# Performance work log

Hardware: AMD Instinct MI355X
Metric: run time of the kernel (lower is better)

The kernel has to match this reference:

```python
import jax, jax.numpy as jnp
import numpy as np

B, T, C, H = 4, 2048, 1024, 16
D = C // H  # head dim = 64

def setup_inputs() -> dict:
    key = jax.random.key(0)
    ks = jax.random.split(key, 5)
    s = 0.02
    return {
        "x": jax.random.normal(ks[0], (B, T, C), dtype=jnp.float32),
        # torch Linear convention: weight shape (out, in), y = x @ W.T + b
        "Wqkv": jax.random.normal(ks[1], (3 * C, C), dtype=jnp.float32) * s,
        "bqkv": jax.random.normal(ks[2], (3 * C,), dtype=jnp.float32) * s,
        "Wproj": jax.random.normal(ks[3], (C, C), dtype=jnp.float32) * s,
        "bproj": jax.random.normal(ks[4], (C,), dtype=jnp.float32) * s,
    }

def reference(x, Wqkv, bqkv, Wproj, bproj):
    b, t, c = x.shape
    qkv = x @ Wqkv.T + bqkv                      # [B,T,3C]
    q, k, v = jnp.split(qkv, 3, axis=-1)
    # [B,T,C] -> [B,H,T,D]
    q = q.reshape(b, t, H, D).transpose(0, 2, 1, 3)
    k = k.reshape(b, t, H, D).transpose(0, 2, 1, 3)
    v = v.reshape(b, t, H, D).transpose(0, 2, 1, 3)
    scale = 1.0 / jnp.sqrt(jnp.float32(D))
    att = jnp.einsum('bhqd,bhkd->bhqk', q, k) * scale   # [B,H,T,T]
    # additive causal mask: -inf strictly above diagonal
    mask = jnp.triu(jnp.full((t, t), -jnp.inf, dtype=att.dtype), k=1)
    att = att + mask
    att = jax.nn.softmax(att, axis=-1)
    # dropout p=0.0 -> identity
    y = jnp.einsum('bhqk,bhkd->bhqd', att, v)            # [B,H,T,D]
    y = y.transpose(0, 2, 1, 3).reshape(b, t, c)         # [B,T,C]
    y = y @ Wproj.T + bproj
    return y
```

## Files before the change

kernel.cpp:

```cpp
#include <hip/hip_runtime.h>
#include <hip/hip_bf16.h>
#include <stdint.h>

constexpr int BB = 4, TT = 2048, CC = 1024, HH = 16, DD = 64;

typedef __bf16 bf16_t;
typedef bf16_t bf16x8 __attribute__((ext_vector_type(8)));
typedef float f32x4 __attribute__((ext_vector_type(4)));

__device__ __forceinline__ unsigned short f2bf(float f) {
    union { __bf16 h; unsigned short u; } v;
    v.h = (__bf16)f;
    return v.u;
}

__device__ __forceinline__ f32x4 mfma16(bf16x8 a, bf16x8 b, f32x4 c) {
    return __builtin_amdgcn_mfma_f32_16x16x32_bf16(a, b, c, 0, 0, 0);
}

#define LOAD_LDS16(g, l)                                                      \
    __builtin_amdgcn_global_load_lds(                                         \
        (const __attribute__((address_space(1))) void*)(g),                   \
        (__attribute__((address_space(3))) void*)(l), 16, 0, 0)

__global__ __launch_bounds__(256) void cvt_bf16(const float* __restrict__ in,
                                                unsigned short* __restrict__ out,
                                                long n) {
    long i = ((long)blockIdx.x * blockDim.x + threadIdx.x) * 4;
    long stride = (long)gridDim.x * blockDim.x * 4;
    for (; i < n; i += stride) {
        float4 v = *(const float4*)(in + i);
        ushort4 o;
        o.x = f2bf(v.x); o.y = f2bf(v.y); o.z = f2bf(v.z); o.w = f2bf(v.w);
        *(ushort4*)(out + i) = o;
    }
}

template <int MODE>
__global__ __launch_bounds__(256, 2) void gemm_bt(
    const unsigned short* __restrict__ A,
    const unsigned short* __restrict__ Bw,
    const float* __restrict__ bias,
    unsigned short* __restrict__ qb, unsigned short* __restrict__ kb,
    unsigned short* __restrict__ vtb, float* __restrict__ outf,
    int M, int N, int K) {
    __shared__ unsigned short As[2][128 * 32];
    __shared__ unsigned short Bs[2][128 * 32];
    const int tid = threadIdx.x;
    const int w = tid >> 6, lane = tid & 63;
    const int g = lane >> 4, q16 = lane & 15;
    const int wr = w >> 1, wc = w & 1;
    const int mbase = blockIdx.x * 128;
    const int nbase = blockIdx.y * 128;
    const int srow = lane >> 2;
    const int scol = (lane & 3) * 8;

    f32x4 acc[4][4];
#pragma unroll
    for (int i = 0; i < 4; ++i)
#pragma unroll
        for (int j = 0; j < 4; ++j) acc[i][j] = (f32x4){0.f, 0.f, 0.f, 0.f};

    const int nk = K >> 5;

    auto stage = [&](int buf, int t) {
        const int k0 = t << 5;
#pragma unroll
        for (int ii = 0; ii < 2; ++ii) {
            const int i = w + ii * 4;
            const unsigned short* ga =
                A + (long)(mbase + i * 16 + srow) * K + k0 + scol;
            LOAD_LDS16(ga, &As[buf][i * 512]);
            const unsigned short* gb =
                Bw + (long)(nbase + i * 16 + srow) * K + k0 + scol;
            LOAD_LDS16(gb, &Bs[buf][i * 512]);
        }
    };

    stage(0, 0);
    __syncthreads();
    int cur = 0;
    for (int t = 0; t < nk; ++t) {
        if (t + 1 < nk) stage(cur ^ 1, t + 1);
        bf16x8 af[4], bfr[4];
#pragma unroll
        for (int mi = 0; mi < 4; ++mi)
            af[mi] = *(const bf16x8*)&As[cur][(wr * 64 + mi * 16 + q16) * 32 + 8 * g];
#pragma unroll
        for (int ni = 0; ni < 4; ++ni)
            bfr[ni] = *(const bf16x8*)&Bs[cur][(wc * 64 + ni * 16 + q16) * 32 + 8 * g];
#pragma unroll
        for (int mi = 0; mi < 4; ++mi)
#pragma unroll
            for (int ni = 0; ni < 4; ++ni)
                acc[mi][ni] = mfma16(af[mi], bfr[ni], acc[mi][ni]);
        __syncthreads();
        cur ^= 1;
    }

#pragma unroll
    for (int mi = 0; mi < 4; ++mi) {
#pragma unroll
        for (int ni = 0; ni < 4; ++ni) {
            const int n = nbase + wc * 64 + ni * 16 + q16;
            const float bv = bias[n];
#pragma unroll
            for (int r = 0; r < 4; ++r) {
                const int m = mbase + wr * 64 + mi * 16 + 4 * g + r;
                const float val = acc[mi][ni][r] + bv;
                if (MODE == 0) {
                    const int which = n >> 10, rem = n & 1023;
                    const int h = rem >> 6, d = rem & 63;
                    const int b = m >> 11, t = m & 2047;
                    const long bh = (long)(b * HH + h);
                    if (which == 0)
                        qb[(bh * TT + t) * DD + d] = f2bf(val * 0.125f);
                    else if (which == 1)
                        kb[(bh * TT + t) * DD + d] = f2bf(val);
                    else
                        vtb[(bh * DD + d) * TT + t] = f2bf(val);
                } else {
                    outf[(long)m * N + n] = val;
                }
            }
        }
    }
}

__global__ __launch_bounds__(256, 4) void attn_fwd(
    const unsigned short* __restrict__ qb, const unsigned short* __restrict__ kb,
    const unsigned short* __restrict__ vtb, unsigned short* __restrict__ attb) {
    __shared__ __align__(16) unsigned short Ks[2][64 * 64];
    __shared__ __align__(16) unsigned short Vs[2][64 * 64];
    __shared__ __align__(16) unsigned short plds[4][16 * 64];
    const int tid = threadIdx.x;
    const int w = tid >> 6, lane = tid & 63;
    const int g = lane >> 4, q16 = lane & 15;
    const int bid = blockIdx.x;
    const int swz = (bid & 7) * 256 + (bid >> 3);
    const int bx = swz & 31, bh = swz >> 5;
    const int b = bh >> 4, h = bh & 15;
    const int qbase = bx * 64 + w * 16;

    const unsigned short* Q = qb + (long)bh * TT * DD;
    const unsigned short* Kp = kb + (long)bh * TT * DD;
    const unsigned short* Vt = vtb + (long)bh * DD * TT;

    const int srow = tid >> 3;
    const int ssl = ((tid & 7) ^ (srow & 7)) * 8;
    unsigned short* kdst0 = &Ks[0][0] + w * 512;
    unsigned short* vdst0 = &Vs[0][0] + w * 512;

    auto stageKV = [&](int buf, int kt) {
        const long kb0 = (long)kt * 64;
        const unsigned short* gk = Kp + (kb0 + srow) * DD + ssl;
        const unsigned short* gv = Vt + (long)srow * TT + kb0 + ssl;
        unsigned short* kd = kdst0 + buf * 4096;
        unsigned short* vd = vdst0 + buf * 4096;
        LOAD_LDS16(gk, kd);
        LOAD_LDS16(gk + 32l * DD, kd + 2048);
        LOAD_LDS16(gv, vd);
        LOAD_LDS16(gv + 32l * TT, vd + 2048);
    };

    bf16x8 aq0 = *(const bf16x8*)&Q[(qbase + q16) * DD + 8 * g];
    bf16x8 aq1 = *(const bf16x8*)&Q[(qbase + q16) * DD + 32 + 8 * g];

    f32x4 acc[4];
#pragma unroll
    for (int i = 0; i < 4; ++i) acc[i] = (f32x4){0.f, 0.f, 0.f, 0.f};
    float mrow = -1e30f, lrow = 0.f;

    const int slot0 = (g ^ (q16 & 7)) << 3;
    const int nkt = bx + 1;
    stageKV(0, 0);
    __syncthreads();
    int cur = 0;
    for (int kt = 0; kt < nkt; ++kt) {
        if (kt + 1 < nkt) stageKV(cur ^ 1, kt + 1);
        const int kbase = kt * 64;
        f32x4 p[4];
#pragma unroll
        for (int s = 0; s < 4; ++s) p[s] = (f32x4){0.f, 0.f, 0.f, 0.f};
#pragma unroll
        for (int s = 0; s < 4; ++s) {
            const int kr = (16 * s + q16) * 64;
            bf16x8 bk0 = *(const bf16x8*)&Ks[cur][kr + slot0];
            bf16x8 bk1 = *(const bf16x8*)&Ks[cur][kr + (slot0 ^ 32)];
            p[s] = mfma16(bk0, aq0, p[s]);
            p[s] = mfma16(bk1, aq1, p[s]);
        }
        const int q = qbase + q16;
        if (kt == nkt - 1) {
#pragma unroll
            for (int s = 0; s < 4; ++s)
#pragma unroll
                for (int r = 0; r < 4; ++r)
                    if (kbase + 16 * s + 4 * g + r > q) p[s][r] = -1e30f;
        }
        float t = fmaxf(fmaxf(p[0][0], p[0][1]), fmaxf(p[0][2], p[0][3]));
#pragma unroll
        for (int s = 1; s < 4; ++s)
            t = fmaxf(t, fmaxf(fmaxf(p[s][0], p[s][1]), fmaxf(p[s][2], p[s][3])));
        t = fmaxf(t, __shfl_xor(t, 16));
        t = fmaxf(t, __shfl_xor(t, 32));
        if (__all(t - mrow <= 8.0f)) {
            float ssum = 0.f;
#pragma unroll
            for (int s = 0; s < 4; ++s)
#pragma unroll
                for (int r = 0; r < 4; ++r) {
                    p[s][r] = __expf(p[s][r] - mrow);
                    ssum += p[s][r];
                }
            ssum += __shfl_xor(ssum, 16);
            ssum += __shfl_xor(ssum, 32);
            lrow += ssum;
        } else {
            const float nm = fmaxf(mrow, t);
            const float fs = __expf(mrow - nm);
            mrow = nm;
            float ssum = 0.f;
#pragma unroll
            for (int s = 0; s < 4; ++s)
#pragma unroll
                for (int r = 0; r < 4; ++r) {
                    p[s][r] = __expf(p[s][r] - nm);
                    ssum += p[s][r];
                }
            ssum += __shfl_xor(ssum, 16);
            ssum += __shfl_xor(ssum, 32);
            lrow = lrow * fs + ssum;
            float fr[4];
#pragma unroll
            for (int r = 0; r < 4; ++r) fr[r] = __shfl(fs, 4 * g + r);
#pragma unroll
            for (int ni = 0; ni < 4; ++ni)
#pragma unroll
                for (int r = 0; r < 4; ++r) acc[ni][r] *= fr[r];
        }
#pragma unroll
        for (int s = 0; s < 4; ++s) {
            ushort4 pk;
            pk.x = f2bf(p[s][0]); pk.y = f2bf(p[s][1]);
            pk.z = f2bf(p[s][2]); pk.w = f2bf(p[s][3]);
            const int Gp = ((2 * s + (g >> 1)) ^ (q16 & 7)) * 8 + (g & 1) * 4;
            *(ushort4*)&plds[w][q16 * 64 + Gp] = pk;
        }
        bf16x8 pa0 = *(const bf16x8*)&plds[w][q16 * 64 + slot0];
        bf16x8 pa1 = *(const bf16x8*)&plds[w][q16 * 64 + (slot0 ^ 32)];
#pragma unroll
        for (int ni = 0; ni < 4; ++ni) {
            const int vr = (ni * 16 + q16) * 64;
            bf16x8 bv0 = *(const bf16x8*)&Vs[cur][vr + slot0];
            bf16x8 bv1 = *(const bf16x8*)&Vs[cur][vr + (slot0 ^ 32)];
            acc[ni] = mfma16(pa0, bv0, acc[ni]);
            acc[ni] = mfma16(pa1, bv1, acc[ni]);
        }
        __syncthreads();
        cur ^= 1;
    }
    float inv[4];
#pragma unroll
    for (int r = 0; r < 4; ++r) inv[r] = 1.0f / __shfl(lrow, 4 * g + r);
#pragma unroll
    for (int ni = 0; ni < 4; ++ni)
#pragma unroll
        for (int r = 0; r < 4; ++r) {
            const int q = qbase + 4 * g + r;
            const int d = ni * 16 + q16;
            attb[(((long)b * TT + q) * HH + h) * DD + d] =
                f2bf(acc[ni][r] * inv[r]);
        }
}

extern "C" void kernel_launch(void* const* d_in, const int* in_sizes, int n_in,
                              void* d_out, int out_size, void* d_ws, size_t ws_size,
                              hipStream_t stream) {
    const float* x = (const float*)d_in[0];
    const float* Wqkv = (const float*)d_in[1];
    const float* bqkv = (const float*)d_in[2];
    const float* Wproj = (const float*)d_in[3];
    const float* bproj = (const float*)d_in[4];
    float* out = (float*)d_out;

    char* ws = (char*)d_ws;
    unsigned short* xb = (unsigned short*)(ws);
    unsigned short* wqkvb = (unsigned short*)(ws + (16l << 20));
    unsigned short* wprojb = (unsigned short*)(ws + (22l << 20));
    unsigned short* qb = (unsigned short*)(ws + (24l << 20));
    unsigned short* kb = (unsigned short*)(ws + (40l << 20));
    unsigned short* vtb = (unsigned short*)(ws + (56l << 20));
    unsigned short* attb = xb;

    cvt_bf16<<<2048, 256, 0, stream>>>(x, xb, (long)BB * TT * CC);
    cvt_bf16<<<2048, 256, 0, stream>>>(Wqkv, wqkvb, (long)3 * CC * CC);
    cvt_bf16<<<1024, 256, 0, stream>>>(Wproj, wprojb, (long)CC * CC);

    gemm_bt<0><<<dim3(64, 24), 256, 0, stream>>>(xb, wqkvb, bqkv, qb, kb, vtb,
                                                 nullptr, BB * TT, 3 * CC, CC);
    attn_fwd<<<2048, 256, 0, stream>>>(qb, kb, vtb, attb);
    gemm_bt<1><<<dim3(64, 8), 256, 0, stream>>>(attb, wprojb, bproj, nullptr,
                                                nullptr, nullptr, out, BB * TT,
                                                CC, CC);
}
```

Measured before the change: 218.9 us.

## Double attention query tile per block, merge conversion kernels, add MFMA priority hints

Each attention block now handles 128 query rows, with each wave owning two 16-row sub-tiles. Every staged K/V tile is therefore reused by twice as many queries, and the grid is halved. The causal mask is now applied per sub-tile whenever the key block crosses the diagonal. The three fp32-to-bf16 conversion launches are merged into one kernel that dispatches by index range, and s_setprio is raised around the MFMA sections. The larger tile costs more registers and gives coarser causal load balance, since the longest blocks now do twice the work.

```diff
diff --git a/kernel.cpp b/kernel.cpp
--- a/kernel.cpp
+++ b/kernel.cpp
@@ -23,16 +23,26 @@
         (const __attribute__((address_space(1))) void*)(g),                   \
         (__attribute__((address_space(3))) void*)(l), 16, 0, 0)
 
-__global__ __launch_bounds__(256) void cvt_bf16(const float* __restrict__ in,
-                                                unsigned short* __restrict__ out,
-                                                long n) {
-    long i = ((long)blockIdx.x * blockDim.x + threadIdx.x) * 4;
-    long stride = (long)gridDim.x * blockDim.x * 4;
-    for (; i < n; i += stride) {
-        float4 v = *(const float4*)(in + i);
+__global__ __launch_bounds__(256) void cvt_all(
+    const float* __restrict__ a, long na,
+    const float* __restrict__ b, long nb,
+    const float* __restrict__ c, long nc,
+    unsigned short* __restrict__ oa, unsigned short* __restrict__ ob,
+    unsigned short* __restrict__ oc) {
+    const long ntot = na + nb + nc;
+    long i = (long)blockIdx.x * blockDim.x + threadIdx.x;
+    const long stride = (long)gridDim.x * blockDim.x;
+    for (; i < ntot; i += stride) {
+        const float* src;
+        unsigned short* dst;
+        long q = i;
+        if (q < na) { src = a; dst = oa; }
+        else if (q < na + nb) { q -= na; src = b; dst = ob; }
+        else { q -= na + nb; src = c; dst = oc; }
+        float4 v = *(const float4*)(src + q * 4);
         ushort4 o;
         o.x = f2bf(v.x); o.y = f2bf(v.y); o.z = f2bf(v.z); o.w = f2bf(v.w);
-        *(ushort4*)(out + i) = o;
+        *(ushort4*)(dst + q * 4) = o;
     }
 }
 
@@ -137,10 +147,10 @@
     const int w = tid >> 6, lane = tid & 63;
     const int g = lane >> 4, q16 = lane & 15;
     const int bid = blockIdx.x;
-    const int swz = (bid & 7) * 256 + (bid >> 3);
-    const int bx = swz & 31, bh = swz >> 5;
+    const int swz = (bid & 7) * 128 + (bid >> 3);
+    const int bx = swz & 15, bh = swz >> 4;
     const int b = bh >> 4, h = bh & 15;
-    const int qbase = bx * 64 + w * 16;
+    const int qbase = bx * 128 + w * 32;
 
     const unsigned short* Q = qb + (long)bh * TT * DD;
     const unsigned short* Kp = kb + (long)bh * TT * DD;
@@ -163,115 +173,132 @@
         LOAD_LDS16(gv + 32l * TT, vd + 2048);
     };
 
-    bf16x8 aq0 = *(const bf16x8*)&Q[(qbase + q16) * DD + 8 * g];
-    bf16x8 aq1 = *(const bf16x8*)&Q[(qbase + q16) * DD + 32 + 8 * g];
-
-    f32x4 acc[4];
-#pragma unroll
-    for (int i = 0; i < 4; ++i) acc[i] = (f32x4){0.f, 0.f, 0.f, 0.f};
-    float mrow = -1e30f, lrow = 0.f;
+    bf16x8 aq[2][2];
+#pragma unroll
+    for (int js = 0; js < 2; ++js) {
+        aq[js][0] = *(const bf16x8*)&Q[(qbase + js * 16 + q16) * DD + 8 * g];
+        aq[js][1] = *(const bf16x8*)&Q[(qbase + js * 16 + q16) * DD + 32 + 8 * g];
+    }
+
+    f32x4 acc[2][4];
+#pragma unroll
+    for (int js = 0; js < 2; ++js)
+#pragma unroll
+        for (int i = 0; i < 4; ++i) acc[js][i] = (f32x4){0.f, 0.f, 0.f, 0.f};
+    float mrow[2] = {-1e30f, -1e30f}, lrow[2] = {0.f, 0.f};
 
     const int slot0 = (g ^ (q16 & 7)) << 3;
-    const int nkt = bx + 1;
+    const int nkt = 2 * bx + 2;
     stageKV(0, 0);
     __syncthreads();
     int cur = 0;
     for (int kt = 0; kt < nkt; ++kt) {
         if (kt + 1 < nkt) stageKV(cur ^ 1, kt + 1);
         const int kbase = kt * 64;
-        f32x4 p[4];
-#pragma unroll
-        for (int s = 0; s < 4; ++s) p[s] = (f32x4){0.f, 0.f, 0.f, 0.f};
-#pragma unroll
-        for (int s = 0; s < 4; ++s) {
-            const int kr = (16 * s + q16) * 64;
-            bf16x8 bk0 = *(const bf16x8*)&Ks[cur][kr + slot0];
-            bf16x8 bk1 = *(const bf16x8*)&Ks[cur][kr + (slot0 ^ 32)];
-            p[s] = mfma16(bk0, aq0, p[s]);
-            p[s] = mfma16(bk1, aq1, p[s]);
-        }
-        const int q = qbase + q16;
-        if (kt == nkt - 1) {
-#pragma unroll
-            for (int s = 0; s < 4; ++s)
-#pragma unroll
-                for (int r = 0; r < 4; ++r)
-                    if (kbase + 16 * s + 4 * g + r > q) p[s][r] = -1e30f;
-        }
-        float t = fmaxf(fmaxf(p[0][0], p[0][1]), fmaxf(p[0][2], p[0][3]));
-#pragma unroll
-        for (int s = 1; s < 4; ++s)
-            t = fmaxf(t, fmaxf(fmaxf(p[s][0], p[s][1]), fmaxf(p[s][2], p[s][3])));
-        t = fmaxf(t, __shfl_xor(t, 16));
-        t = fmaxf(t, __shfl_xor(t, 32));
-        if (__all(t - mrow <= 8.0f)) {
-            float ssum = 0.f;
-#pragma unroll
-            for (int s = 0; s < 4; ++s)
-#pragma unroll
-                for (int r = 0; r < 4; ++r) {
-                    p[s][r] = __expf(p[s][r] - mrow);
-                    ssum += p[s][r];
-                }
-            ssum += __shfl_xor(ssum, 16);
-            ssum += __shfl_xor(ssum, 32);
-            lrow += ssum;
-        } else {
-            const float nm = fmaxf(mrow, t);
-            const float fs = __expf(mrow - nm);
-            mrow = nm;
-            float ssum = 0.f;
-#pragma unroll
-            for (int s = 0; s < 4; ++s)
-#pragma unroll
-                for (int r = 0; r < 4; ++r) {
-                    p[s][r] = __expf(p[s][r] - nm);
-                    ssum += p[s][r];
-                }
-            ssum += __shfl_xor(ssum, 16);
-            ssum += __shfl_xor(ssum, 32);
-            lrow = lrow * fs + ssum;
-            float fr[4];
-#pragma unroll
-            for (int r = 0; r < 4; ++r) fr[r] = __shfl(fs, 4 * g + r);
-#pragma unroll
-            for (int ni = 0; ni < 4; ++ni)
-#pragma unroll
-                for (int r = 0; r < 4; ++r) acc[ni][r] *= fr[r];
-        }
-#pragma unroll
-        for (int s = 0; s < 4; ++s) {
-            ushort4 pk;
-            pk.x = f2bf(p[s][0]); pk.y = f2bf(p[s][1]);
-            pk.z = f2bf(p[s][2]); pk.w = f2bf(p[s][3]);
-            const int Gp = ((2 * s + (g >> 1)) ^ (q16 & 7)) * 8 + (g & 1) * 4;
-            *(ushort4*)&plds[w][q16 * 64 + Gp] = pk;
-        }
-        bf16x8 pa0 = *(const bf16x8*)&plds[w][q16 * 64 + slot0];
-        bf16x8 pa1 = *(const bf16x8*)&plds[w][q16 * 64 + (slot0 ^ 32)];
-#pragma unroll
-        for (int ni = 0; ni < 4; ++ni) {
-            const int vr = (ni * 16 + q16) * 64;
-            bf16x8 bv0 = *(const bf16x8*)&Vs[cur][vr + slot0];
-            bf16x8 bv1 = *(const bf16x8*)&Vs[cur][vr + (slot0 ^ 32)];
-            acc[ni] = mfma16(pa0, bv0, acc[ni]);
-            acc[ni] = mfma16(pa1, bv1, acc[ni]);
+#pragma unroll
+        for (int js = 0; js < 2; ++js) {
+            f32x4 p[4];
+#pragma unroll
+            for (int s = 0; s < 4; ++s) p[s] = (f32x4){0.f, 0.f, 0.f, 0.f};
+            __builtin_amdgcn_s_setprio(1);
+#pragma unroll
+            for (int s = 0; s < 4; ++s) {
+                const int kr = (16 * s + q16) * 64;
+                bf16x8 bk0 = *(const bf16x8*)&Ks[cur][kr + slot0];
+                bf16x8 bk1 = *(const bf16x8*)&Ks[cur][kr + (slot0 ^ 32)];
+                p[s] = mfma16(bk0, aq[js][0], p[s]);
+                p[s] = mfma16(bk1, aq[js][1], p[s]);
+            }
+            __builtin_amdgcn_s_setprio(0);
+            const int qset = qbase + js * 16;
+            if (kbase + 63 > qset) {
+                const int q = qset + q16;
+#pragma unroll
+                for (int s = 0; s < 4; ++s)
+#pragma unroll
+                    for (int r = 0; r < 4; ++r)
+                        if (kbase + 16 * s + 4 * g + r > q) p[s][r] = -1e30f;
+            }
+            float t = fmaxf(fmaxf(p[0][0], p[0][1]), fmaxf(p[0][2], p[0][3]));
+#pragma unroll
+            for (int s = 1; s < 4; ++s)
+                t = fmaxf(t, fmaxf(fmaxf(p[s][0], p[s][1]), fmaxf(p[s][2], p[s][3])));
+            t = fmaxf(t, __shfl_xor(t, 16));
+            t = fmaxf(t, __shfl_xor(t, 32));
+            if (__all(t - mrow[js] <= 8.0f)) {
+                float ssum = 0.f;
+#pragma unroll
+                for (int s = 0; s < 4; ++s)
+#pragma unroll
+                    for (int r = 0; r < 4; ++r) {
+                        p[s][r] = __expf(p[s][r] - mrow[js]);
+                        ssum += p[s][r];
+                    }
+                ssum += __shfl_xor(ssum, 16);
+                ssum += __shfl_xor(ssum, 32);
+                lrow[js] += ssum;
+            } else {
+                const float nm = fmaxf(mrow[js], t);
+                const float fs = __expf(mrow[js] - nm);
+                mrow[js] = nm;
+                float ssum = 0.f;
+#pragma unroll
+                for (int s = 0; s < 4; ++s)
+#pragma unroll
+                    for (int r = 0; r < 4; ++r) {
+                        p[s][r] = __expf(p[s][r] - nm);
+                        ssum += p[s][r];
+                    }
+                ssum += __shfl_xor(ssum, 16);
+                ssum += __shfl_xor(ssum, 32);
+                lrow[js] = lrow[js] * fs + ssum;
+                float fr[4];
+#pragma unroll
+                for (int r = 0; r < 4; ++r) fr[r] = __shfl(fs, 4 * g + r);
+#pragma unroll
+                for (int ni = 0; ni < 4; ++ni)
+#pragma unroll
+                    for (int r = 0; r < 4; ++r) acc[js][ni][r] *= fr[r];
+            }
+#pragma unroll
+            for (int s = 0; s < 4; ++s) {
+                ushort4 pk;
+                pk.x = f2bf(p[s][0]); pk.y = f2bf(p[s][1]);
+                pk.z = f2bf(p[s][2]); pk.w = f2bf(p[s][3]);
+                const int Gp = ((2 * s + (g >> 1)) ^ (q16 & 7)) * 8 + (g & 1) * 4;
+                *(ushort4*)&plds[w][q16 * 64 + Gp] = pk;
+            }
+            bf16x8 pa0 = *(const bf16x8*)&plds[w][q16 * 64 + slot0];
+            bf16x8 pa1 = *(const bf16x8*)&plds[w][q16 * 64 + (slot0 ^ 32)];
+            __builtin_amdgcn_s_setprio(1);
+#pragma unroll
+            for (int ni = 0; ni < 4; ++ni) {
+                const int vr = (ni * 16 + q16) * 64;
+                bf16x8 bv0 = *(const bf16x8*)&Vs[cur][vr + slot0];
+                bf16x8 bv1 = *(const bf16x8*)&Vs[cur][vr + (slot0 ^ 32)];
+                acc[js][ni] = mfma16(pa0, bv0, acc[js][ni]);
+                acc[js][ni] = mfma16(pa1, bv1, acc[js][ni]);
+            }
+            __builtin_amdgcn_s_setprio(0);
         }
         __syncthreads();
         cur ^= 1;
     }
-    float inv[4];
-#pragma unroll
-    for (int r = 0; r < 4; ++r) inv[r] = 1.0f / __shfl(lrow, 4 * g + r);
-#pragma unroll
-    for (int ni = 0; ni < 4; ++ni)
-#pragma unroll
-        for (int r = 0; r < 4; ++r) {
-            const int q = qbase + 4 * g + r;
-            const int d = ni * 16 + q16;
-            attb[(((long)b * TT + q) * HH + h) * DD + d] =
-                f2bf(acc[ni][r] * inv[r]);
-        }
+#pragma unroll
+    for (int js = 0; js < 2; ++js) {
+        float inv[4];
+#pragma unroll
+        for (int r = 0; r < 4; ++r) inv[r] = 1.0f / __shfl(lrow[js], 4 * g + r);
+#pragma unroll
+        for (int ni = 0; ni < 4; ++ni)
+#pragma unroll
+            for (int r = 0; r < 4; ++r) {
+                const int q = qbase + js * 16 + 4 * g + r;
+                const int d = ni * 16 + q16;
+                attb[(((long)b * TT + q) * HH + h) * DD + d] =
+                    f2bf(acc[js][ni][r] * inv[r]);
+            }
+    }
 }
 
 extern "C" void kernel_launch(void* const* d_in, const int* in_sizes, int n_in,
@@ -293,13 +320,13 @@
     unsigned short* vtb = (unsigned short*)(ws + (56l << 20));
     unsigned short* attb = xb;
 
-    cvt_bf16<<<2048, 256, 0, stream>>>(x, xb, (long)BB * TT * CC);
-    cvt_bf16<<<2048, 256, 0, stream>>>(Wqkv, wqkvb, (long)3 * CC * CC);
-    cvt_bf16<<<1024, 256, 0, stream>>>(Wproj, wprojb, (long)CC * CC);
+    cvt_all<<<2048, 256, 0, stream>>>(
+        x, (long)BB * TT * CC / 4, Wqkv, (long)3 * CC * CC / 4, Wproj,
+        (long)CC * CC / 4, xb, wqkvb, wprojb);
 
     gemm_bt<0><<<dim3(64, 24), 256, 0, stream>>>(xb, wqkvb, bqkv, qb, kb, vtb,
                                                  nullptr, BB * TT, 3 * CC, CC);
-    attn_fwd<<<2048, 256, 0, stream>>>(qb, kb, vtb, attb);
+    attn_fwd<<<1024, 256, 0, stream>>>(qb, kb, vtb, attb);
     gemm_bt<1><<<dim3(64, 8), 256, 0, stream>>>(attb, wprojb, bproj, nullptr,
                                                 nullptr, nullptr, out, BB * TT,
                                                 CC, CC);
```

Result: slower. 288.6 us (+31.8%).

## Use 256x256-tile 8-wave QKV GEMM with swizzled LDS and fused conversion kernel

Applied to the files above, without the earlier changes.

Replaces the 128x128 QKV projection GEMM with a 512-thread, 256x256-tile kernel. It uses XOR-swizzled LDS staging, interleaved half-tile prefetch under s_waitcnt control, setprio around MFMA bursts, and XCD-aware block swizzling. It also merges the three fp32-to-bf16 conversion launches into one kernel, and keeps a separate simpler kernel for the output projection. The larger tile is meant to raise arithmetic intensity and cut global reloads, but it only yields 384 workgroups and raises register and LDS pressure.

```diff
diff --git a/kernel.cpp b/kernel.cpp
--- a/kernel.cpp
+++ b/kernel.cpp
@@ -23,27 +23,185 @@
         (const __attribute__((address_space(1))) void*)(g),                   \
         (__attribute__((address_space(3))) void*)(l), 16, 0, 0)
 
-__global__ __launch_bounds__(256) void cvt_bf16(const float* __restrict__ in,
-                                                unsigned short* __restrict__ out,
-                                                long n) {
-    long i = ((long)blockIdx.x * blockDim.x + threadIdx.x) * 4;
-    long stride = (long)gridDim.x * blockDim.x * 4;
-    for (; i < n; i += stride) {
-        float4 v = *(const float4*)(in + i);
+__global__ __launch_bounds__(256) void cvt_all(
+    const float* __restrict__ a, long na,
+    const float* __restrict__ b, long nb,
+    const float* __restrict__ c, long nc,
+    unsigned short* __restrict__ oa, unsigned short* __restrict__ ob,
+    unsigned short* __restrict__ oc) {
+    const long ntot = na + nb + nc;
+    long i = (long)blockIdx.x * blockDim.x + threadIdx.x;
+    const long stride = (long)gridDim.x * blockDim.x;
+    for (; i < ntot; i += stride) {
+        const float* src;
+        unsigned short* dst;
+        long q = i;
+        if (q < na) { src = a; dst = oa; }
+        else if (q < na + nb) { q -= na; src = b; dst = ob; }
+        else { q -= na + nb; src = c; dst = oc; }
+        float4 v = *(const float4*)(src + q * 4);
         ushort4 o;
         o.x = f2bf(v.x); o.y = f2bf(v.y); o.z = f2bf(v.z); o.w = f2bf(v.w);
-        *(ushort4*)(out + i) = o;
-    }
-}
-
-template <int MODE>
-__global__ __launch_bounds__(256, 2) void gemm_bt(
+        *(ushort4*)(dst + q * 4) = o;
+    }
+}
+
+__global__ __launch_bounds__(512, 2) void gemm256_qkv(
     const unsigned short* __restrict__ A,
     const unsigned short* __restrict__ Bw,
     const float* __restrict__ bias,
     unsigned short* __restrict__ qb, unsigned short* __restrict__ kb,
-    unsigned short* __restrict__ vtb, float* __restrict__ outf,
-    int M, int N, int K) {
+    unsigned short* __restrict__ vtb, int M, int N, int K) {
+    __shared__ unsigned short As[2][2][256 * 32];
+    __shared__ unsigned short Bs[2][2][256 * 32];
+    const int tid = threadIdx.x;
+    const int w = tid >> 6, lane = tid & 63;
+    const int g = lane >> 4, q16 = lane & 15;
+    const int wr = w >> 2, wc = w & 3;
+
+    const int nwg = (M >> 8) * (N >> 8);
+    const int cpx = nwg >> 3;
+    const int bid = blockIdx.x;
+    const int swz = (bid & 7) * cpx + (bid >> 3);
+    const int ntiles = N >> 8;
+    const int mtile = swz / ntiles, ntile = swz % ntiles;
+    const int mbase = mtile << 8, nbase = ntile << 8;
+
+    f32x4 acc[8][4];
+#pragma unroll
+    for (int i = 0; i < 8; ++i)
+#pragma unroll
+        for (int j = 0; j < 4; ++j) acc[i][j] = (f32x4){0.f, 0.f, 0.f, 0.f};
+
+    const int strow = w * 16 + (lane >> 2);
+    const int stsl = ((lane & 3) ^ ((lane >> 3) & 3)) * 8;
+    auto stage_half = [&](unsigned short* dstb, const unsigned short* srcrow0) {
+#pragma unroll
+        for (int i = 0; i < 2; ++i) {
+            const unsigned short* src =
+                srcrow0 + (long)(i * 128 + strow) * 1024 + stsl;
+            LOAD_LDS16(src, dstb + i * 4096 + w * 512);
+        }
+    };
+
+    const int rsl = (g ^ ((q16 >> 1) & 3)) * 8;
+    auto dsA = [&](bf16x8* fr, int mi0, int kh, int buf) {
+#pragma unroll
+        for (int i = 0; i < 4; ++i) {
+            const int row = wr * 128 + (mi0 + i) * 16 + q16;
+            fr[i] = *(const bf16x8*)&As[buf][kh][row * 32 + rsl];
+        }
+    };
+    auto dsB = [&](bf16x8* fr, int kh, int buf) {
+#pragma unroll
+        for (int i = 0; i < 4; ++i) {
+            const int row = wc * 64 + i * 16 + q16;
+            fr[i] = *(const bf16x8*)&Bs[buf][kh][row * 32 + rsl];
+        }
+    };
+
+    const unsigned short* Ag = A + (long)mbase * K;
+    const unsigned short* Bg = Bw + (long)nbase * K;
+
+    stage_half(&As[0][0][0], Ag);
+    stage_half(&Bs[0][0][0], Bg);
+    stage_half(&As[0][1][0], Ag + 32);
+    stage_half(&Bs[0][1][0], Bg + 32);
+    asm volatile("s_waitcnt vmcnt(0)" ::: "memory");
+    __builtin_amdgcn_s_barrier();
+
+    const int NT = K >> 6;
+    bf16x8 af[4], bfr[4];
+    for (int t = 0; t < NT; ++t) {
+        const int buf = t & 1, nbuf = buf ^ 1;
+        const bool hasNext = (t + 1 < NT);
+        const long kn = (long)(t + 1) * 64;
+        dsA(af, 0, 0, buf);
+        dsB(bfr, 0, buf);
+        if (hasNext) stage_half(&As[nbuf][0][0], Ag + kn);
+        __builtin_amdgcn_s_barrier();
+        __builtin_amdgcn_s_setprio(1);
+#pragma unroll
+        for (int i = 0; i < 4; ++i)
+#pragma unroll
+            for (int j = 0; j < 4; ++j)
+                acc[i][j] = mfma16(af[i], bfr[j], acc[i][j]);
+        __builtin_amdgcn_s_setprio(0);
+        __builtin_amdgcn_s_barrier();
+        dsA(af, 4, 0, buf);
+        if (hasNext) {
+            stage_half(&Bs[nbuf][0][0], Bg + kn);
+            asm volatile("s_waitcnt vmcnt(4)" ::: "memory");
+        } else {
+            asm volatile("s_waitcnt vmcnt(0)" ::: "memory");
+        }
+        __builtin_amdgcn_s_barrier();
+        __builtin_amdgcn_s_setprio(1);
+#pragma unroll
+        for (int i = 0; i < 4; ++i)
+#pragma unroll
+            for (int j = 0; j < 4; ++j)
+                acc[4 + i][j] = mfma16(af[i], bfr[j], acc[4 + i][j]);
+        __builtin_amdgcn_s_setprio(0);
+        __builtin_amdgcn_s_barrier();
+        dsA(af, 0, 1, buf);
+        dsB(bfr, 1, buf);
+        if (hasNext) stage_half(&As[nbuf][1][0], Ag + kn + 32);
+        __builtin_amdgcn_s_barrier();
+        __builtin_amdgcn_s_setprio(1);
+#pragma unroll
+        for (int i = 0; i < 4; ++i)
+#pragma unroll
+            for (int j = 0; j < 4; ++j)
+                acc[i][j] = mfma16(af[i], bfr[j], acc[i][j]);
+        __builtin_amdgcn_s_setprio(0);
+        __builtin_amdgcn_s_barrier();
+        dsA(af, 4, 1, buf);
+        if (hasNext) {
+            stage_half(&Bs[nbuf][1][0], Bg + kn + 32);
+            asm volatile("s_waitcnt vmcnt(4)" ::: "memory");
+        }
+        __builtin_amdgcn_s_barrier();
+        __builtin_amdgcn_s_setprio(1);
+#pragma unroll
+        for (int i = 0; i < 4; ++i)
+#pragma unroll
+            for (int j = 0; j < 4; ++j)
+                acc[4 + i][j] = mfma16(af[i], bfr[j], acc[4 + i][j]);
+        __builtin_amdgcn_s_setprio(0);
+        __builtin_amdgcn_s_barrier();
+    }
+
+#pragma unroll
+    for (int mi = 0; mi < 8; ++mi) {
+#pragma unroll
+        for (int ni = 0; ni < 4; ++ni) {
+            const int n = nbase + wc * 64 + ni * 16 + q16;
+            const float bv = bias[n];
+#pragma unroll
+            for (int r = 0; r < 4; ++r) {
+                const int m = mbase + wr * 128 + mi * 16 + 4 * g + r;
+                const float val = acc[mi][ni][r] + bv;
+                const int which = n >> 10, rem = n & 1023;
+                const int h = rem >> 6, d = rem & 63;
+                const int b = m >> 11, t = m & 2047;
+                const long bh = (long)(b * HH + h);
+                if (which == 0)
+                    qb[(bh * TT + t) * DD + d] = f2bf(val * 0.125f);
+                else if (which == 1)
+                    kb[(bh * TT + t) * DD + d] = f2bf(val);
+                else
+                    vtb[(bh * DD + d) * TT + t] = f2bf(val);
+            }
+        }
+    }
+}
+
+__global__ __launch_bounds__(256, 2) void gemm_proj(
+    const unsigned short* __restrict__ A,
+    const unsigned short* __restrict__ Bw,
+    const float* __restrict__ bias,
+    float* __restrict__ outf, int M, int N, int K) {
     __shared__ unsigned short As[2][128 * 32];
     __shared__ unsigned short Bs[2][128 * 32];
     const int tid = threadIdx.x;
@@ -107,21 +265,7 @@
 #pragma unroll
             for (int r = 0; r < 4; ++r) {
                 const int m = mbase + wr * 64 + mi * 16 + 4 * g + r;
-                const float val = acc[mi][ni][r] + bv;
-                if (MODE == 0) {
-                    const int which = n >> 10, rem = n & 1023;
-                    const int h = rem >> 6, d = rem & 63;
-                    const int b = m >> 11, t = m & 2047;
-                    const long bh = (long)(b * HH + h);
-                    if (which == 0)
-                        qb[(bh * TT + t) * DD + d] = f2bf(val * 0.125f);
-                    else if (which == 1)
-                        kb[(bh * TT + t) * DD + d] = f2bf(val);
-                    else
-                        vtb[(bh * DD + d) * TT + t] = f2bf(val);
-                } else {
-                    outf[(long)m * N + n] = val;
-                }
+                outf[(long)m * N + n] = acc[mi][ni][r] + bv;
             }
         }
     }
@@ -293,14 +437,13 @@
     unsigned short* vtb = (unsigned short*)(ws + (56l << 20));
     unsigned short* attb = xb;
 
-    cvt_bf16<<<2048, 256, 0, stream>>>(x, xb, (long)BB * TT * CC);
-    cvt_bf16<<<2048, 256, 0, stream>>>(Wqkv, wqkvb, (long)3 * CC * CC);
-    cvt_bf16<<<1024, 256, 0, stream>>>(Wproj, wprojb, (long)CC * CC);
-
-    gemm_bt<0><<<dim3(64, 24), 256, 0, stream>>>(xb, wqkvb, bqkv, qb, kb, vtb,
-                                                 nullptr, BB * TT, 3 * CC, CC);
+    cvt_all<<<2048, 256, 0, stream>>>(
+        x, (long)BB * TT * CC / 4, Wqkv, (long)3 * CC * CC / 4, Wproj,
+        (long)CC * CC / 4, xb, wqkvb, wprojb);
+
+    gemm256_qkv<<<384, 512, 0, stream>>>(xb, wqkvb, bqkv, qb, kb, vtb,
+                                         BB * TT, 3 * CC, CC);
     attn_fwd<<<2048, 256, 0, stream>>>(qb, kb, vtb, attb);
-    gemm_bt<1><<<dim3(64, 8), 256, 0, stream>>>(attb, wprojb, bproj, nullptr,
-                                                nullptr, nullptr, out, BB * TT,
-                                                CC, CC);
-}
+    gemm_proj<<<dim3(64, 8), 256, 0, stream>>>(attb, wprojb, bproj, out,
+                                               BB * TT, CC, CC);
+}
```

Result: slower. 224.2 us (+2.4%).
